# Kernel optimization log

Hardware: AMD Instinct MI355X
Metric: run time of the kernel (lower is better)

Reference implementation:

```python
import jax, jax.numpy as jnp
import numpy as np

B, T, C, HD = 4, 2048, 1024, 64

def setup_inputs() -> dict:
    key = jax.random.key(0)
    kx, kq, kk, kv = jax.random.split(key, 4)
    # Weights stored as [n_embed, head_size]; equivalent to torch Linear weight transposed.
    scale = 1.0 / np.sqrt(C)
    return {
        "x": jax.random.normal(kx, (B, T, C), dtype=jnp.float32),
        "Wq": jax.random.normal(kq, (C, HD), dtype=jnp.float32) * scale,
        "Wk": jax.random.normal(kk, (C, HD), dtype=jnp.float32) * scale,
        "Wv": jax.random.normal(kv, (C, HD), dtype=jnp.float32) * scale,
    }

def reference(x, Wq, Wk, Wv):
    # Projections (no bias)
    q = x @ Wq  # [B,T,HD]
    k = x @ Wk
    v = x @ Wv
    hd = k.shape[-1]
    # NOTE: original multiplies by sqrt(head_size) (not the usual 1/sqrt) -- faithful.
    scores = jnp.einsum("btd,bsd->bts", q, k) * (hd ** 0.5)  # [B,T,T]
    # First softmax over full (unmasked) rows
    w = jax.nn.softmax(scores, axis=-1)
    # Causal mask applied AFTER the first softmax, then a second softmax
    causal = jnp.tril(jnp.ones((q.shape[1], q.shape[1]), dtype=bool))  # [T,T]
    w = jnp.where(causal[None, :, :], w, -jnp.inf)
    w = jax.nn.softmax(w, axis=-1)
    out = jnp.einsum("bts,bsd->btd", w, v)  # [B,T,HD]
    return out
```

## Files before the change

### kernel.cpp

```cpp
#include <hip/hip_runtime.h>
#include <math.h>

#define T_  2048
#define C_  1024
#define HD_ 64

typedef __attribute__((ext_vector_type(8))) short bf16x8;
typedef __attribute__((ext_vector_type(4))) float f32x4;

#define MFMA_BF16(A, B, C) __builtin_amdgcn_mfma_f32_16x16x32_bf16(A, B, C, 0, 0, 0)

__device__ __forceinline__ short f2bf(float f) {
    union { float f; unsigned u; } v; v.f = f;
    unsigned r = v.u + 0x7fffu + ((v.u >> 16) & 1u);
    return (short)(r >> 16);
}
__device__ __forceinline__ float bf2f(short s) {
    union { float f; unsigned u; } v;
    v.u = ((unsigned)(unsigned short)s) << 16;
    return v.f;
}

__global__ __launch_bounds__(256) void prep_w_kernel(
    const float* __restrict__ Wq, const float* __restrict__ Wk,
    const float* __restrict__ Wv, short* __restrict__ wtf)
{
    const int m = blockIdx.y;
    const float* W = (m == 0) ? Wq : (m == 1) ? Wk : Wv;
    const int t = threadIdx.x;
    const int c = blockIdx.x * 64 + (t >> 2);
    const int hg = (t & 3) * 16;
    const int ct = m * 4 + (t & 3);
    const int c0i = c >> 6, kc = (c >> 5) & 1, lq = (c >> 3) & 3, e = c & 7;
    const float4* wp = (const float4*)(W + (size_t)c * HD_ + hg);
    #pragma unroll
    for (int u = 0; u < 4; ++u) {
        float4 f = wp[u];
        float vs[4] = {f.x, f.y, f.z, f.w};
        #pragma unroll
        for (int ei = 0; ei < 4; ++ei) {
            int h16 = u * 4 + ei;
            int L = h16 + 16 * lq;
            short hh = f2bf(vs[ei]);
            short lo = f2bf(vs[ei] - bf2f(hh));
            size_t oh = ((((size_t)(ct * 2 + 0) * 16 + c0i) * 2 + kc) * 64 + L) * 8 + e;
            size_t ol = ((((size_t)(ct * 2 + 1) * 16 + c0i) * 2 + kc) * 64 + L) * 8 + e;
            wtf[oh] = hh;
            wtf[ol] = lo;
        }
    }
}

__global__ __launch_bounds__(256) void qkv_proj_kernel(
    const float* __restrict__ x, const short* __restrict__ wtf,
    short* __restrict__ qhp, short* __restrict__ qlp,
    short* __restrict__ khp, short* __restrict__ klp,
    short* __restrict__ vtp)
{
    __shared__ __align__(16) short xh[2][16 * 64], xl[2][16 * 64];

    const int t = threadIdx.x, L = t & 63, wv = t >> 6;
    const int R0 = blockIdx.x * 16;
    const int ctq = wv;

    f32x4 acc[3];
    #pragma unroll
    for (int j = 0; j < 3; ++j) acc[j] = {0.f, 0.f, 0.f, 0.f};

    const int xrow = t >> 4, xc4 = t & 15;
    const float* xp = x + (size_t)(R0 + xrow) * C_ + xc4 * 4;
    float4 xa;
    auto loadX = [&](int c0) { xa = *(const float4*)(xp + c0); };

    const int c8 = xc4 >> 1, xhalf = xc4 & 1;
    const int slot = xrow * 64 + ((c8 ^ (xrow & 7)) * 8) + xhalf * 4;
    auto stageX = [&](int buf) {
        float vs[4] = {xa.x, xa.y, xa.z, xa.w};
        short4 vh, vl;
        short* vhp = (short*)&vh; short* vlp = (short*)&vl;
        #pragma unroll
        for (int e = 0; e < 4; ++e) {
            short hh = f2bf(vs[e]);
            vhp[e] = hh;
            vlp[e] = f2bf(vs[e] - bf2f(hh));
        }
        *(short4*)&xh[buf][slot] = vh;
        *(short4*)&xl[buf][slot] = vl;
    };

    const size_t lo8 = (size_t)L * 8;
    auto loadWF = [&](int c0i, int kc, bf16x8* w) {
        w[0] = *(const bf16x8*)(wtf + (size_t)((((ctq + 0) * 2 + 0) * 16 + c0i) * 2 + kc) * 512 + lo8);
        w[1] = *(const bf16x8*)(wtf + (size_t)((((ctq + 0) * 2 + 1) * 16 + c0i) * 2 + kc) * 512 + lo8);
        w[2] = *(const bf16x8*)(wtf + (size_t)((((ctq + 4) * 2 + 0) * 16 + c0i) * 2 + kc) * 512 + lo8);
        w[3] = *(const bf16x8*)(wtf + (size_t)((((ctq + 4) * 2 + 1) * 16 + c0i) * 2 + kc) * 512 + lo8);
        w[4] = *(const bf16x8*)(wtf + (size_t)((((ctq + 8) * 2 + 0) * 16 + c0i) * 2 + kc) * 512 + lo8);
    };

    bf16x8 wf0[5], wf1[5];
    const int arow = L & 15;

    loadX(0);
    loadWF(0, 0, wf0);
    stageX(0);
    loadX(64);
    __syncthreads();

    for (int c0i = 0; c0i < 16; ++c0i) {
        const int cur = c0i & 1;
        if (c0i < 15) {
            stageX(cur ^ 1);
            if (c0i < 14) loadX((c0i + 2) * 64);
        }
        loadWF(c0i, 1, wf1);
        {
            int ch = 0 * 4 + (L >> 4);
            int off = arow * 64 + ((ch ^ (arow & 7)) * 8);
            bf16x8 axh = *(const bf16x8*)&xh[cur][off];
            bf16x8 axl = *(const bf16x8*)&xl[cur][off];
            acc[0] = MFMA_BF16(axl, wf0[0], acc[0]);
            acc[0] = MFMA_BF16(axh, wf0[1], acc[0]);
            acc[0] = MFMA_BF16(axh, wf0[0], acc[0]);
            acc[1] = MFMA_BF16(axl, wf0[2], acc[1]);
            acc[1] = MFMA_BF16(axh, wf0[3], acc[1]);
            acc[1] = MFMA_BF16(axh, wf0[2], acc[1]);
            acc[2] = MFMA_BF16(wf0[4], axh, acc[2]);
        }
        if (c0i < 15) loadWF(c0i + 1, 0, wf0);
        {
            int ch = 1 * 4 + (L >> 4);
            int off = arow * 64 + ((ch ^ (arow & 7)) * 8);
            bf16x8 axh = *(const bf16x8*)&xh[cur][off];
            bf16x8 axl = *(const bf16x8*)&xl[cur][off];
            acc[0] = MFMA_BF16(axl, wf1[0], acc[0]);
            acc[0] = MFMA_BF16(axh, wf1[1], acc[0]);
            acc[0] = MFMA_BF16(axh, wf1[0], acc[0]);
            acc[1] = MFMA_BF16(axl, wf1[2], acc[1]);
            acc[1] = MFMA_BF16(axh, wf1[3], acc[1]);
            acc[1] = MFMA_BF16(axh, wf1[2], acc[1]);
            acc[2] = MFMA_BF16(wf1[4], axh, acc[2]);
        }
        __syncthreads();
    }

    const int quad = L >> 4;
    #pragma unroll
    for (int r = 0; r < 4; ++r) {
        int row = R0 + quad * 4 + r;
        int h = ctq * 16 + (L & 15);
        float vq = acc[0][r] * 8.f;
        short hq = f2bf(vq);
        qhp[(size_t)row * HD_ + h] = hq;
        qlp[(size_t)row * HD_ + h] = f2bf(vq - bf2f(hq));
        float vk = acc[1][r];
        short hk = f2bf(vk);
        khp[(size_t)row * HD_ + h] = hk;
        klp[(size_t)row * HD_ + h] = f2bf(vk - bf2f(hk));
        int d = ctq * 16 + quad * 4 + r;
        int tt = R0 + (L & 15);
        int bb = tt >> 11, tl = tt & (T_ - 1);
        vtp[(size_t)(bb * 64 + d) * T_ + tl] = f2bf(acc[2][r]);
    }
}

__global__ __launch_bounds__(256) void stats_kernel(
    const short* __restrict__ qhp, const short* __restrict__ qlp,
    const short* __restrict__ khp, const short* __restrict__ klp,
    float* __restrict__ pm, float* __restrict__ sc)
{
    __shared__ float red[4 * 64 * 2];

    const int t = threadIdx.x, L = t & 63, wv = t >> 6;
    const int bt = blockIdx.x, seg = blockIdx.y, b = blockIdx.z;
    const int R0 = bt * 64, S0 = seg * 256;

    bf16x8 qfh[4][2], qfl[4][2];
    #pragma unroll
    for (int rt = 0; rt < 4; ++rt)
        #pragma unroll
        for (int dc = 0; dc < 2; ++dc) {
            int row = R0 + rt * 16 + (L & 15);
            size_t off = ((size_t)b * T_ + row) * HD_ + dc * 32 + (L >> 4) * 8;
            qfh[rt][dc] = *(const bf16x8*)(qhp + off);
            qfl[rt][dc] = *(const bf16x8*)(qlp + off);
        }

    float ml[4][4], ll[4][4];
    #pragma unroll
    for (int rt = 0; rt < 4; ++rt)
        #pragma unroll
        for (int r = 0; r < 4; ++r) { ml[rt][r] = -1e30f; ll[rt][r] = 0.f; }

    const int colL = wv * 16 + (L & 15);
    const short* kbh = khp + ((size_t)b * T_ + S0 + colL) * HD_;
    const short* kbl = klp + ((size_t)b * T_ + S0 + colL) * HD_;
    const int cho = (L >> 4) * 8;

    bf16x8 kfh[2][2], kfl[2][2];
    auto loadK = [&](int jt, bf16x8 kh[2], bf16x8 kl[2]) {
        #pragma unroll
        for (int dc = 0; dc < 2; ++dc) {
            kh[dc] = *(const bf16x8*)(kbh + (size_t)jt * 64 * HD_ + dc * 32 + cho);
            kl[dc] = *(const bf16x8*)(kbl + (size_t)jt * 64 * HD_ + dc * 32 + cho);
        }
    };
    loadK(0, kfh[0], kfl[0]);

    #pragma unroll
    for (int jt = 0; jt < 4; ++jt) {
        const int cb = jt & 1;
        if (jt < 3) loadK(jt + 1, kfh[cb ^ 1], kfl[cb ^ 1]);
        const bool doStore = (S0 + jt * 64) <= (R0 + 63);
        #pragma unroll
        for (int rt = 0; rt < 4; ++rt) {
            f32x4 s = {0.f, 0.f, 0.f, 0.f};
            #pragma unroll
            for (int dc = 0; dc < 2; ++dc) {
                s = MFMA_BF16(qfl[rt][dc], kfh[cb][dc], s);
                s = MFMA_BF16(qfh[rt][dc], kfl[cb][dc], s);
                s = MFMA_BF16(qfh[rt][dc], kfh[cb][dc], s);
            }
            if (doStore) {
                #pragma unroll
                for (int r = 0; r < 4; ++r) {
                    int row = R0 + rt * 16 + (L >> 4) * 4 + r;
                    sc[((size_t)b * T_ + row) * T_ + S0 + jt * 64 + colL] = s[r];
                }
            }
            #pragma unroll
            for (int r = 0; r < 4; ++r) {
                float mn = fmaxf(ml[rt][r], s[r]);
                ll[rt][r] = ll[rt][r] * __expf(ml[rt][r] - mn) + __expf(s[r] - mn);
                ml[rt][r] = mn;
            }
        }
    }
    #pragma unroll
    for (int off = 1; off < 16; off <<= 1)
        #pragma unroll
        for (int rt = 0; rt < 4; ++rt)
            #pragma unroll
            for (int r = 0; r < 4; ++r) {
                float mo = __shfl_xor(ml[rt][r], off, 64);
                float lo = __shfl_xor(ll[rt][r], off, 64);
                float mn = fmaxf(ml[rt][r], mo);
                ll[rt][r] = ll[rt][r] * __expf(ml[rt][r] - mn) + lo * __expf(mo - mn);
                ml[rt][r] = mn;
            }
    if ((L & 15) == 0) {
        #pragma unroll
        for (int rt = 0; rt < 4; ++rt)
            #pragma unroll
            for (int r = 0; r < 4; ++r) {
                int row = rt * 16 + (L >> 4) * 4 + r;
                red[(wv * 64 + row) * 2 + 0] = ml[rt][r];
                red[(wv * 64 + row) * 2 + 1] = ll[rt][r];
            }
    }
    __syncthreads();
    if (t < 64) {
        float M = red[t * 2], S = red[t * 2 + 1];
        #pragma unroll
        for (int w = 1; w < 4; ++w) {
            float mo = red[(w * 64 + t) * 2], lo = red[(w * 64 + t) * 2 + 1];
            float mn = fmaxf(M, mo);
            S = S * __expf(M - mn) + lo * __expf(mo - mn);
            M = mn;
        }
        size_t o = ((size_t)((b * 32 + bt) * 8 + seg) * 64 + t) * 2;
        pm[o] = M;
        pm[o + 1] = S;
    }
}

__global__ __launch_bounds__(256) void pv_kernel(
    const float* __restrict__ sc, const short* __restrict__ vtp,
    const float* __restrict__ pm, float* __restrict__ out)
{
    __shared__ float ored[4][16][64];
    __shared__ float dred[4][16];
    __shared__ float msl[16];

    const int t = threadIdx.x, L = t & 63, wv = t >> 6;
    const int b = blockIdx.x & 3;
    const int i = blockIdx.x >> 2;
    const int p = (i < 64) ? (127 - i) : (i - 64);
    const int T0 = p * 16;

    if (t < 16) {
        int row = T0 + t;
        int bt = row >> 6, rr = row & 63;
        float M = -1e30f, S = 0.f;
        #pragma unroll
        for (int seg = 0; seg < 8; ++seg) {
            size_t o = ((size_t)((b * 32 + bt) * 8 + seg) * 64 + rr) * 2;
            float mo = pm[o], lo = pm[o + 1];
            float mn = fmaxf(M, mo);
            S = S * __expf(M - mn) + lo * __expf(mo - mn);
            M = mn;
        }
        msl[t] = M + __logf(S);
    }
    __syncthreads();

    const int row = T0 + (L & 15);
    const float mls = msl[L & 15];
    const float* srow = sc + ((size_t)b * T_ + row) * T_;
    const short* vb = vtp + (size_t)b * 64 * T_;
    const int nJ = (T0 + 143) >> 7;
    const int cq = (L >> 4) * 8;

    f32x4 ov[4];
    #pragma unroll
    for (int dt = 0; dt < 4; ++dt) ov[dt] = {0.f, 0.f, 0.f, 0.f};
    float dn = 0.f;

    float4 sa0, sa1, sb0, sb1;
    bf16x8 va0, va1, va2, va3, vb0, vb1, vb2, vb3;

#define LDS_(jt, s0, s1) { int c0_ = (jt) * 128 + wv * 32 + cq;                  \
        s0 = *(const float4*)(srow + c0_); s1 = *(const float4*)(srow + c0_ + 4); }
#define LDV_(jt, v0, v1, v2, v3) { int c0_ = (jt) * 128 + wv * 32 + cq;          \
        v0 = *(const bf16x8*)(vb + (size_t)( 0 + (L & 15)) * T_ + c0_);          \
        v1 = *(const bf16x8*)(vb + (size_t)(16 + (L & 15)) * T_ + c0_);          \
        v2 = *(const bf16x8*)(vb + (size_t)(32 + (L & 15)) * T_ + c0_);          \
        v3 = *(const bf16x8*)(vb + (size_t)(48 + (L & 15)) * T_ + c0_); }
#define BODY_(jt, s0, s1, v0, v1, v2, v3) {                                      \
        const int c0_ = (jt) * 128 + wv * 32 + cq;                               \
        float vs_[8] = {s0.x, s0.y, s0.z, s0.w, s1.x, s1.y, s1.z, s1.w};         \
        bf16x8 ef_;                                                              \
        _Pragma("unroll")                                                        \
        for (int e = 0; e < 8; ++e) {                                            \
            float pvv = __expf(vs_[e] - mls);                                    \
            float evv = (c0_ + e <= row) ? __expf(pvv) : 0.f;                    \
            dn += evv;                                                           \
            ef_[e] = f2bf(evv);                                                  \
        }                                                                        \
        ov[0] = MFMA_BF16(ef_, v0, ov[0]);                                       \
        ov[1] = MFMA_BF16(ef_, v1, ov[1]);                                       \
        ov[2] = MFMA_BF16(ef_, v2, ov[2]);                                       \
        ov[3] = MFMA_BF16(ef_, v3, ov[3]); }

    LDS_(0, sa0, sa1)
    LDV_(0, va0, va1, va2, va3)
    int jt = 0;
    for (; jt + 2 <= nJ; jt += 2) {
        LDS_(jt + 1, sb0, sb1)
        LDV_(jt + 1, vb0, vb1, vb2, vb3)
        BODY_(jt, sa0, sa1, va0, va1, va2, va3)
        if (jt + 2 < nJ) {
            LDS_(jt + 2, sa0, sa1)
            LDV_(jt + 2, va0, va1, va2, va3)
        }
        BODY_(jt + 1, sb0, sb1, vb0, vb1, vb2, vb3)
    }
    if (jt < nJ) {
        BODY_(jt, sa0, sa1, va0, va1, va2, va3)
    }
#undef LDS_
#undef LDV_
#undef BODY_

    dn += __shfl_xor(dn, 16, 64);
    dn += __shfl_xor(dn, 32, 64);
    if (L < 16) dred[wv][L] = dn;
    #pragma unroll
    for (int dt = 0; dt < 4; ++dt)
        #pragma unroll
        for (int r = 0; r < 4; ++r)
            ored[wv][(L >> 4) * 4 + r][dt * 16 + (L & 15)] = ov[dt][r];
    __syncthreads();

    const int orow = t >> 4, d0 = (t & 15) * 4;
    float D = dred[0][orow] + dred[1][orow] + dred[2][orow] + dred[3][orow];
    float di = 1.f / D;
    float4 o;
    o.x = (ored[0][orow][d0 + 0] + ored[1][orow][d0 + 0]
         + ored[2][orow][d0 + 0] + ored[3][orow][d0 + 0]) * di;
    o.y = (ored[0][orow][d0 + 1] + ored[1][orow][d0 + 1]
         + ored[2][orow][d0 + 1] + ored[3][orow][d0 + 1]) * di;
    o.z = (ored[0][orow][d0 + 2] + ored[1][orow][d0 + 2]
         + ored[2][orow][d0 + 2] + ored[3][orow][d0 + 2]) * di;
    o.w = (ored[0][orow][d0 + 3] + ored[1][orow][d0 + 3]
         + ored[2][orow][d0 + 3] + ored[3][orow][d0 + 3]) * di;
    *(float4*)(out + ((size_t)b * T_ + T0 + orow) * HD_ + d0) = o;
}

extern "C" void kernel_launch(void* const* d_in, const int* in_sizes, int n_in,
                              void* d_out, int out_size, void* d_ws, size_t ws_size,
                              hipStream_t stream) {
    (void)in_sizes; (void)n_in; (void)out_size; (void)ws_size;
    const float* x  = (const float*)d_in[0];
    const float* Wq = (const float*)d_in[1];
    const float* Wk = (const float*)d_in[2];
    const float* Wv = (const float*)d_in[3];
    float* outp = (float*)d_out;

    char* ws = (char*)d_ws;
    short* wt  = (short*)ws;
    float* pm  = (float*)ws;
    short* qh = (short*)(ws + 786432);
    short* ql = (short*)(ws + 786432 + 1048576);
    short* kh = (short*)(ws + 786432 + 2 * 1048576);
    short* kl = (short*)(ws + 786432 + 3 * 1048576);
    short* vt = (short*)(ws + 786432 + 4 * 1048576);
    float* sc = (float*)(ws + 8388608);

    prep_w_kernel<<<dim3(16, 3), 256, 0, stream>>>(Wq, Wk, Wv, wt);
    qkv_proj_kernel<<<dim3(512), 256, 0, stream>>>(x, wt, qh, ql, kh, kl, vt);
    stats_kernel<<<dim3(32, 8, 4), 256, 0, stream>>>(qh, ql, kh, kl, pm, sc);
    pv_kernel<<<dim3(512), 256, 0, stream>>>(sc, vt, pm, outp);
}
```

Measured before the change: 135.1 us.

## Use base-2 exponentials, batch stats reductions, and widen QKV projection tiles

```diff
diff --git a/kernel.cpp b/kernel.cpp
--- a/kernel.cpp
+++ b/kernel.cpp
@@ -9,6 +9,10 @@
 typedef __attribute__((ext_vector_type(4))) float f32x4;
 
 #define MFMA_BF16(A, B, C) __builtin_amdgcn_mfma_f32_16x16x32_bf16(A, B, C, 0, 0, 0)
+
+#define QSCALE 11.54156032711171f
+
+#define EXP2F(x) __builtin_amdgcn_exp2f(x)
 
 __device__ __forceinline__ short f2bf(float f) {
     union { float f; unsigned u; } v; v.f = f;
@@ -51,17 +55,18 @@
     }
 }
 
-__global__ __launch_bounds__(256) void qkv_proj_kernel(
+__global__ __launch_bounds__(512) void qkv_proj_kernel(
     const float* __restrict__ x, const short* __restrict__ wtf,
     short* __restrict__ qhp, short* __restrict__ qlp,
     short* __restrict__ khp, short* __restrict__ klp,
     short* __restrict__ vtp)
 {
-    __shared__ __align__(16) short xh[2][16 * 64], xl[2][16 * 64];
+    __shared__ __align__(16) short xh[2][32 * 64], xl[2][32 * 64];
 
     const int t = threadIdx.x, L = t & 63, wv = t >> 6;
-    const int R0 = blockIdx.x * 16;
-    const int ctq = wv;
+    const int R0 = blockIdx.x * 32;
+    const int rtb = (wv >> 2) * 16;
+    const int ctq = wv & 3;
 
     f32x4 acc[3];
     #pragma unroll
@@ -98,10 +103,11 @@
     };
 
     bf16x8 wf0[5], wf1[5];
-    const int arow = L & 15;
+    const int arow = rtb + (L & 15);
 
     loadX(0);
     loadWF(0, 0, wf0);
+    loadWF(0, 1, wf1);
     stageX(0);
     loadX(64);
     __syncthreads();
@@ -112,9 +118,8 @@
             stageX(cur ^ 1);
             if (c0i < 14) loadX((c0i + 2) * 64);
         }
-        loadWF(c0i, 1, wf1);
         {
-            int ch = 0 * 4 + (L >> 4);
+            int ch = (L >> 4);
             int off = arow * 64 + ((ch ^ (arow & 7)) * 8);
             bf16x8 axh = *(const bf16x8*)&xh[cur][off];
             bf16x8 axl = *(const bf16x8*)&xl[cur][off];
@@ -128,7 +133,7 @@
         }
         if (c0i < 15) loadWF(c0i + 1, 0, wf0);
         {
-            int ch = 1 * 4 + (L >> 4);
+            int ch = 4 + (L >> 4);
             int off = arow * 64 + ((ch ^ (arow & 7)) * 8);
             bf16x8 axh = *(const bf16x8*)&xh[cur][off];
             bf16x8 axl = *(const bf16x8*)&xl[cur][off];
@@ -140,15 +145,16 @@
             acc[1] = MFMA_BF16(axh, wf1[2], acc[1]);
             acc[2] = MFMA_BF16(wf1[4], axh, acc[2]);
         }
+        if (c0i < 15) loadWF(c0i + 1, 1, wf1);
         __syncthreads();
     }
 
     const int quad = L >> 4;
     #pragma unroll
     for (int r = 0; r < 4; ++r) {
-        int row = R0 + quad * 4 + r;
+        int row = R0 + rtb + quad * 4 + r;
         int h = ctq * 16 + (L & 15);
-        float vq = acc[0][r] * 8.f;
+        float vq = acc[0][r] * QSCALE;
         short hq = f2bf(vq);
         qhp[(size_t)row * HD_ + h] = hq;
         qlp[(size_t)row * HD_ + h] = f2bf(vq - bf2f(hq));
@@ -157,7 +163,7 @@
         khp[(size_t)row * HD_ + h] = hk;
         klp[(size_t)row * HD_ + h] = f2bf(vk - bf2f(hk));
         int d = ctq * 16 + quad * 4 + r;
-        int tt = R0 + (L & 15);
+        int tt = R0 + rtb + (L & 15);
         int bb = tt >> 11, tl = tt & (T_ - 1);
         vtp[(size_t)(bb * 64 + d) * T_ + tl] = f2bf(acc[2][r]);
     }
@@ -185,12 +191,6 @@
             qfl[rt][dc] = *(const bf16x8*)(qlp + off);
         }
 
-    float ml[4][4], ll[4][4];
-    #pragma unroll
-    for (int rt = 0; rt < 4; ++rt)
-        #pragma unroll
-        for (int r = 0; r < 4; ++r) { ml[rt][r] = -1e30f; ll[rt][r] = 0.f; }
-
     const int colL = wv * 16 + (L & 15);
     const short* kbh = khp + ((size_t)b * T_ + S0 + colL) * HD_;
     const short* kbl = klp + ((size_t)b * T_ + S0 + colL) * HD_;
@@ -206,6 +206,7 @@
     };
     loadK(0, kfh[0], kfl[0]);
 
+    f32x4 sv[4][4];
     #pragma unroll
     for (int jt = 0; jt < 4; ++jt) {
         const int cb = jt & 1;
@@ -220,6 +221,7 @@
                 s = MFMA_BF16(qfh[rt][dc], kfl[cb][dc], s);
                 s = MFMA_BF16(qfh[rt][dc], kfh[cb][dc], s);
             }
+            sv[jt][rt] = s;
             if (doStore) {
                 #pragma unroll
                 for (int r = 0; r < 4; ++r) {
@@ -227,14 +229,22 @@
                     sc[((size_t)b * T_ + row) * T_ + S0 + jt * 64 + colL] = s[r];
                 }
             }
-            #pragma unroll
-            for (int r = 0; r < 4; ++r) {
-                float mn = fmaxf(ml[rt][r], s[r]);
-                ll[rt][r] = ll[rt][r] * __expf(ml[rt][r] - mn) + __expf(s[r] - mn);
-                ml[rt][r] = mn;
-            }
-        }
-    }
+        }
+    }
+
+    float ml[4][4], ll[4][4];
+    #pragma unroll
+    for (int rt = 0; rt < 4; ++rt)
+        #pragma unroll
+        for (int r = 0; r < 4; ++r) {
+            float v0 = sv[0][rt][r], v1 = sv[1][rt][r];
+            float v2 = sv[2][rt][r], v3 = sv[3][rt][r];
+            float m = fmaxf(fmaxf(v0, v1), fmaxf(v2, v3));
+            float l = EXP2F(v0 - m) + EXP2F(v1 - m)
+                    + EXP2F(v2 - m) + EXP2F(v3 - m);
+            ml[rt][r] = m; ll[rt][r] = l;
+        }
+
     #pragma unroll
     for (int off = 1; off < 16; off <<= 1)
         #pragma unroll
@@ -244,7 +254,7 @@
                 float mo = __shfl_xor(ml[rt][r], off, 64);
                 float lo = __shfl_xor(ll[rt][r], off, 64);
                 float mn = fmaxf(ml[rt][r], mo);
-                ll[rt][r] = ll[rt][r] * __expf(ml[rt][r] - mn) + lo * __expf(mo - mn);
+                ll[rt][r] = ll[rt][r] * EXP2F(ml[rt][r] - mn) + lo * EXP2F(mo - mn);
                 ml[rt][r] = mn;
             }
     if ((L & 15) == 0) {
@@ -264,7 +274,7 @@
         for (int w = 1; w < 4; ++w) {
             float mo = red[(w * 64 + t) * 2], lo = red[(w * 64 + t) * 2 + 1];
             float mn = fmaxf(M, mo);
-            S = S * __expf(M - mn) + lo * __expf(mo - mn);
+            S = S * EXP2F(M - mn) + lo * EXP2F(mo - mn);
             M = mn;
         }
         size_t o = ((size_t)((b * 32 + bt) * 8 + seg) * 64 + t) * 2;
@@ -296,10 +306,10 @@
             size_t o = ((size_t)((b * 32 + bt) * 8 + seg) * 64 + rr) * 2;
             float mo = pm[o], lo = pm[o + 1];
             float mn = fmaxf(M, mo);
-            S = S * __expf(M - mn) + lo * __expf(mo - mn);
+            S = S * EXP2F(M - mn) + lo * EXP2F(mo - mn);
             M = mn;
         }
-        msl[t] = M + __logf(S);
+        msl[t] = M + __log2f(S);
     }
     __syncthreads();
 
@@ -331,7 +341,7 @@
         bf16x8 ef_;                                                              \
         _Pragma("unroll")                                                        \
         for (int e = 0; e < 8; ++e) {                                            \
-            float pvv = __expf(vs_[e] - mls);                                    \
+            float pvv = EXP2F(vs_[e] - mls);                                     \
             float evv = (c0_ + e <= row) ? __expf(pvv) : 0.f;                    \
             dn += evv;                                                           \
             ef_[e] = f2bf(evv);                                                  \
@@ -407,7 +417,7 @@
     float* sc = (float*)(ws + 8388608);
 
     prep_w_kernel<<<dim3(16, 3), 256, 0, stream>>>(Wq, Wk, Wv, wt);
-    qkv_proj_kernel<<<dim3(512), 256, 0, stream>>>(x, wt, qh, ql, kh, kl, vt);
+    qkv_proj_kernel<<<dim3(256), 512, 0, stream>>>(x, wt, qh, ql, kh, kl, vt);
     stats_kernel<<<dim3(32, 8, 4), 256, 0, stream>>>(qh, ql, kh, kl, pm, sc);
     pv_kernel<<<dim3(512), 256, 0, stream>>>(sc, vt, pm, outp);
 }
```

Result: no change. 136.6 us (+1.1%).
